# Kernel optimization log

Measured on AMD Instinct MI355X. Metric: run time of the kernel, lower is better.

## Reference

```python
import jax, jax.numpy as jnp
import numpy as np

B, NTX, S, OFDM, FFT = 16, 1, 4, 14, 1024   # batch, num_tx, streams, ofdm symbols, subcarriers
NRX, NRXA, T = 4, 1, 16                      # num_rx, rx antennas each, tx antennas


def setup_inputs() -> dict:
    key = jax.random.key(0)
    k = jax.random.split(key, 4)
    return {
        "x_real": jax.random.normal(k[0], (B, NTX, S, OFDM, FFT), jnp.float32),
        "x_imag": jax.random.normal(k[1], (B, NTX, S, OFDM, FFT), jnp.float32),
        "h_real": jax.random.normal(k[2], (B, NRX, NRXA, NTX, T, OFDM, FFT), jnp.float32),
        "h_imag": jax.random.normal(k[3], (B, NRX, NRXA, NTX, T, OFDM, FFT), jnp.float32),
        "precoding_ind": jnp.arange(S, dtype=jnp.int32),  # rx index per stream
    }


def _zero_forcing(x, h):
    # x: [..., S], h: [..., S, T]
    h_herm = jnp.conj(jnp.swapaxes(h, -1, -2))          # [..., T, S]
    hh_herm = jnp.matmul(h, h_herm)                     # [..., S, S] (tiny Gram matrix)
    g = jnp.matmul(h_herm, jnp.linalg.inv(hh_herm))     # [..., T, S] ZF precoder
    x_precoded = jnp.matmul(g, x[..., None])[..., 0]    # [..., T]
    return x_precoded, g


def reference(x_real, x_imag, h_real, h_imag, precoding_ind):
    x = (x_real + 1j * x_imag).astype(jnp.complex64)    # [B, NTX, S, OFDM, FFT]
    h = (h_real + 1j * h_imag).astype(jnp.complex64)    # [B, NRX, NRXA, NTX, T, OFDM, FFT]

    # x.permute(0,1,3,4,2): streams last
    x_p = jnp.transpose(x, (0, 1, 3, 4, 2))             # [B, NTX, OFDM, FFT, S]

    # h.permute(3,1,2,4,5,6,0)
    h_pc = jnp.transpose(h, (3, 1, 2, 4, 5, 6, 0))      # [NTX, NRX, NRXA, T, OFDM, FFT, B]
    # gather desired receivers along num_rx axis
    h_des = h_pc[:, precoding_ind]                      # [NTX, S, NRXA, T, OFDM, FFT, B]
    sh = h_des.shape
    # flatten_dims(., 2, 3): merge rx_ant into tx_ant axis (NRXA=1)
    h_des = h_des.reshape(sh[0], sh[1], sh[2] * sh[3], sh[4], sh[5], sh[6])
    # permute(5,0,3,4,1,2)
    h_des = jnp.transpose(h_des, (5, 0, 3, 4, 1, 2))    # [B, NTX, OFDM, FFT, S, T]

    x_precoded, g = _zero_forcing(x_p, h_des)           # [B, NTX, OFDM, FFT, T]
    # permute(0,1,4,2,3)
    return jnp.transpose(x_precoded, (0, 1, 4, 2, 3))   # [B, NTX, T, OFDM, FFT]
```

## Files before the change

kernel.cpp:

```cpp
#include <hip/hip_runtime.h>
#include <hip/hip_bf16.h>

#define NB    16
#define NS    4
#define NT    16
#define NOFDM 14
#define NFFT  1024
#define SITE  (NOFDM * NFFT)
#define NSITES (NB * SITE)
#define BLK   64

__device__ __forceinline__ unsigned short bf16_bits(float f) {
    unsigned int u = __float_as_uint(f);
    return (unsigned short)((u + 0x7FFFu + ((u >> 16) & 1u)) >> 16);
}

template <int MODE>
__global__ __launch_bounds__(BLK, 2)
void zf_precoder_kernel(
    const float* __restrict__ xr, const float* __restrict__ xi,
    const float* __restrict__ hr, const float* __restrict__ hi,
    void* __restrict__ out_raw)
{
    const int gid = blockIdx.x * BLK + threadIdx.x;
    const int b   = gid / SITE;
    const int rem = gid - b * SITE;

    float Hr[NS][NT], Hi[NS][NT];
    const int hbase = b * (NS * NT * SITE) + rem;
    #pragma unroll
    for (int s = 0; s < NS; ++s) {
        #pragma unroll
        for (int t = 0; t < NT; ++t) {
            const int idx = hbase + (s * NT + t) * SITE;
            Hr[s][t] = hr[idx];
            Hi[s][t] = hi[idx];
        }
    }

    float Xr[NS], Xi[NS];
    const int xbase = b * (NS * SITE) + rem;
    #pragma unroll
    for (int s = 0; s < NS; ++s) {
        Xr[s] = xr[xbase + s * SITE];
        Xi[s] = xi[xbase + s * SITE];
    }

    float Ar[NS][NS], Ai[NS][NS];
    #pragma unroll
    for (int i = 0; i < NS; ++i) {
        #pragma unroll
        for (int j = 0; j <= i; ++j) {
            float sr = 0.f, si = 0.f;
            #pragma unroll
            for (int t = 0; t < NT; ++t) {
                sr += Hr[i][t] * Hr[j][t] + Hi[i][t] * Hi[j][t];
                si += Hi[i][t] * Hr[j][t] - Hr[i][t] * Hi[j][t];
            }
            Ar[i][j] = sr;
            Ai[i][j] = si;
        }
    }

    float invd[NS];
    #pragma unroll
    for (int j = 0; j < NS; ++j) {
        float s = Ar[j][j];
        #pragma unroll
        for (int k = 0; k < j; ++k)
            s -= Ar[j][k] * Ar[j][k] + Ai[j][k] * Ai[j][k];
        const float inv = 1.0f / sqrtf(fmaxf(s, 1e-20f));
        invd[j] = inv;
        #pragma unroll
        for (int i = j + 1; i < NS; ++i) {
            float sr = Ar[i][j], si = Ai[i][j];
            #pragma unroll
            for (int k = 0; k < j; ++k) {
                sr -= Ar[i][k] * Ar[j][k] + Ai[i][k] * Ai[j][k];
                si -= Ai[i][k] * Ar[j][k] - Ar[i][k] * Ai[j][k];
            }
            Ar[i][j] = sr * inv;
            Ai[i][j] = si * inv;
        }
    }

    float Wr[NS], Wi[NS];
    #pragma unroll
    for (int i = 0; i < NS; ++i) {
        float sr = Xr[i], si = Xi[i];
        #pragma unroll
        for (int k = 0; k < i; ++k) {
            sr -= Ar[i][k] * Wr[k] - Ai[i][k] * Wi[k];
            si -= Ar[i][k] * Wi[k] + Ai[i][k] * Wr[k];
        }
        Wr[i] = sr * invd[i];
        Wi[i] = si * invd[i];
    }

    float Zr[NS], Zi[NS];
    #pragma unroll
    for (int i = NS - 1; i >= 0; --i) {
        float sr = Wr[i], si = Wi[i];
        #pragma unroll
        for (int k = i + 1; k < NS; ++k) {
            sr -= Ar[k][i] * Zr[k] + Ai[k][i] * Zi[k];
            si -= Ar[k][i] * Zi[k] - Ai[k][i] * Zr[k];
        }
        Zr[i] = sr * invd[i];
        Zi[i] = si * invd[i];
    }

    const int obase = b * (NT * SITE) + rem;
    #pragma unroll
    for (int t = 0; t < NT; ++t) {
        float yr = 0.f, yi = 0.f;
        #pragma unroll
        for (int s = 0; s < NS; ++s) {
            yr += Hr[s][t] * Zr[s] + Hi[s][t] * Zi[s];
            yi += Hr[s][t] * Zi[s] - Hi[s][t] * Zr[s];
        }
        if (MODE == 0) {
            ((float*)out_raw)[obase + t * SITE] = yr;
        } else {
            ((unsigned int*)out_raw)[obase + t * SITE] =
                (unsigned int)bf16_bits(yr) | ((unsigned int)bf16_bits(yi) << 16);
        }
    }
}

extern "C" void kernel_launch(void* const* d_in, const int* in_sizes, int n_in,
                              void* d_out, int out_size, void* d_ws, size_t ws_size,
                              hipStream_t stream) {
    const float* xr = (const float*)d_in[0];
    const float* xi = (const float*)d_in[1];
    const float* hr = (const float*)d_in[2];
    const float* hi = (const float*)d_in[3];

    const int grid = NSITES / BLK;
    if (out_size == NB * NT * SITE) {
        zf_precoder_kernel<0><<<grid, BLK, 0, stream>>>(xr, xi, hr, hi, d_out);
    } else {
        zf_precoder_kernel<1><<<grid, BLK, 0, stream>>>(xr, xi, hr, hi, d_out);
    }
}
```

Before: 27.71 us.

## Stage channel matrix into LDS via direct global_load_lds instead of registers

```diff
diff --git a/kernel.cpp b/kernel.cpp
--- a/kernel.cpp
+++ b/kernel.cpp
@@ -8,58 +8,85 @@
 #define NFFT  1024
 #define SITE  (NOFDM * NFFT)
 #define NSITES (NB * SITE)
-#define BLK   64
+#define NPL   (NS * NT)
 
 __device__ __forceinline__ unsigned short bf16_bits(float f) {
     unsigned int u = __float_as_uint(f);
     return (unsigned short)((u + 0x7FFFu + ((u >> 16) & 1u)) >> 16);
 }
 
+__device__ __forceinline__ void load_lds16(const float* g, float* lds_uniform_base) {
+    __builtin_amdgcn_global_load_lds(
+        (const __attribute__((address_space(1))) unsigned int*)g,
+        (__attribute__((address_space(3))) unsigned int*)lds_uniform_base,
+        16, 0, 0);
+}
+
 template <int MODE>
-__global__ __launch_bounds__(BLK, 2)
+__global__ __launch_bounds__(64)
 void zf_precoder_kernel(
     const float* __restrict__ xr, const float* __restrict__ xi,
     const float* __restrict__ hr, const float* __restrict__ hi,
     void* __restrict__ out_raw)
 {
-    const int gid = blockIdx.x * BLK + threadIdx.x;
-    const int b   = gid / SITE;
-    const int rem = gid - b * SITE;
+    __shared__ float Hre[NPL * 64];
+    __shared__ float Him[NPL * 64];
 
-    float Hr[NS][NT], Hi[NS][NT];
-    const int hbase = b * (NS * NT * SITE) + rem;
-    #pragma unroll
-    for (int s = 0; s < NS; ++s) {
-        #pragma unroll
-        for (int t = 0; t < NT; ++t) {
-            const int idx = hbase + (s * NT + t) * SITE;
-            Hr[s][t] = hr[idx];
-            Hi[s][t] = hi[idx];
-        }
-    }
+    const int l     = threadIdx.x;
+    const int site0 = blockIdx.x * 64;
+    const int b     = site0 / SITE;
+    const int rem0  = site0 - b * SITE;
 
     float Xr[NS], Xi[NS];
-    const int xbase = b * (NS * SITE) + rem;
+    const int xbase = b * (NS * SITE) + rem0 + l;
     #pragma unroll
     for (int s = 0; s < NS; ++s) {
         Xr[s] = xr[xbase + s * SITE];
         Xi[s] = xi[xbase + s * SITE];
     }
 
+    const int hbase    = b * (NPL * SITE) + rem0;
+    const int sliceoff = (l >> 4) * SITE + (l & 15) * 4;
+    const float* gr = hr + hbase + sliceoff;
+    const float* gi = hi + hbase + sliceoff;
+    #pragma unroll
+    for (int k = 0; k < 16; ++k) {
+        load_lds16(gr, &Hre[k * 256]);
+        load_lds16(gi, &Him[k * 256]);
+        gr += 4 * SITE;
+        gi += 4 * SITE;
+    }
+    asm volatile("s_waitcnt vmcnt(0)" ::: "memory");
+
     float Ar[NS][NS], Ai[NS][NS];
-    #pragma unroll
-    for (int i = 0; i < NS; ++i) {
+    {
+        float n0 = 0.f, n1 = 0.f, n2 = 0.f, n3 = 0.f;
+        float r10 = 0.f, i10 = 0.f, r20 = 0.f, i20 = 0.f, r21 = 0.f, i21 = 0.f;
+        float r30 = 0.f, i30 = 0.f, r31 = 0.f, i31 = 0.f, r32 = 0.f, i32 = 0.f;
         #pragma unroll
-        for (int j = 0; j <= i; ++j) {
-            float sr = 0.f, si = 0.f;
-            #pragma unroll
-            for (int t = 0; t < NT; ++t) {
-                sr += Hr[i][t] * Hr[j][t] + Hi[i][t] * Hi[j][t];
-                si += Hi[i][t] * Hr[j][t] - Hr[i][t] * Hi[j][t];
-            }
-            Ar[i][j] = sr;
-            Ai[i][j] = si;
+        for (int t = 0; t < NT; ++t) {
+            const float h0r = Hre[(0 * NT + t) * 64 + l], h0i = Him[(0 * NT + t) * 64 + l];
+            const float h1r = Hre[(1 * NT + t) * 64 + l], h1i = Him[(1 * NT + t) * 64 + l];
+            const float h2r = Hre[(2 * NT + t) * 64 + l], h2i = Him[(2 * NT + t) * 64 + l];
+            const float h3r = Hre[(3 * NT + t) * 64 + l], h3i = Him[(3 * NT + t) * 64 + l];
+            n0 += h0r * h0r + h0i * h0i;
+            n1 += h1r * h1r + h1i * h1i;
+            n2 += h2r * h2r + h2i * h2i;
+            n3 += h3r * h3r + h3i * h3i;
+            r10 += h1r * h0r + h1i * h0i;  i10 += h1i * h0r - h1r * h0i;
+            r20 += h2r * h0r + h2i * h0i;  i20 += h2i * h0r - h2r * h0i;
+            r21 += h2r * h1r + h2i * h1i;  i21 += h2i * h1r - h2r * h1i;
+            r30 += h3r * h0r + h3i * h0i;  i30 += h3i * h0r - h3r * h0i;
+            r31 += h3r * h1r + h3i * h1i;  i31 += h3i * h1r - h3r * h1i;
+            r32 += h3r * h2r + h3i * h2i;  i32 += h3i * h2r - h3r * h2i;
         }
+        Ar[0][0] = n0; Ar[1][1] = n1; Ar[2][2] = n2; Ar[3][3] = n3;
+        Ar[1][0] = r10; Ai[1][0] = i10;
+        Ar[2][0] = r20; Ai[2][0] = i20;
+        Ar[2][1] = r21; Ai[2][1] = i21;
+        Ar[3][0] = r30; Ai[3][0] = i30;
+        Ar[3][1] = r31; Ai[3][1] = i31;
+        Ar[3][2] = r32; Ai[3][2] = i32;
     }
 
     float invd[NS];
@@ -110,19 +137,22 @@
         Zi[i] = si * invd[i];
     }
 
-    const int obase = b * (NT * SITE) + rem;
+    const int obase = b * (NT * SITE) + rem0 + l;
     #pragma unroll
     for (int t = 0; t < NT; ++t) {
         float yr = 0.f, yi = 0.f;
         #pragma unroll
         for (int s = 0; s < NS; ++s) {
-            yr += Hr[s][t] * Zr[s] + Hi[s][t] * Zi[s];
-            yi += Hr[s][t] * Zi[s] - Hi[s][t] * Zr[s];
+            const float hrv = Hre[(s * NT + t) * 64 + l];
+            const float hiv = Him[(s * NT + t) * 64 + l];
+            yr += hrv * Zr[s] + hiv * Zi[s];
+            if (MODE == 1) yi += hrv * Zi[s] - hiv * Zr[s];
         }
+        const int o = obase + t * SITE;
         if (MODE == 0) {
-            ((float*)out_raw)[obase + t * SITE] = yr;
+            ((float*)out_raw)[o] = yr;
         } else {
-            ((unsigned int*)out_raw)[obase + t * SITE] =
+            ((unsigned int*)out_raw)[o] =
                 (unsigned int)bf16_bits(yr) | ((unsigned int)bf16_bits(yi) << 16);
         }
     }
@@ -136,10 +166,10 @@
     const float* hr = (const float*)d_in[2];
     const float* hi = (const float*)d_in[3];
 
-    const int grid = NSITES / BLK;
+    const int grid = NSITES / 64;
     if (out_size == NB * NT * SITE) {
-        zf_precoder_kernel<0><<<grid, BLK, 0, stream>>>(xr, xi, hr, hi, d_out);
+        zf_precoder_kernel<0><<<grid, 64, 0, stream>>>(xr, xi, hr, hi, d_out);
     } else {
-        zf_precoder_kernel<1><<<grid, BLK, 0, stream>>>(xr, xi, hr, hi, d_out);
+        zf_precoder_kernel<1><<<grid, 64, 0, stream>>>(xr, xi, hr, hi, d_out);
     }
 }
```

Measured after the change: 34.84 us. 25.7% more time.
